# Kernel optimization log

Hardware: AMD Instinct MI355X
Metric: run time of the kernel (lower is better)

## Reference

```python
import jax, jax.numpy as jnp
import numpy as np

B, T, D = 8, 768, 1024
H = 16
DH = D // H  # 64, RoPE dim per head
ROPE_BASE = 10000.0


def _rope_tables(length, dim, dtype):
    # (T, dim) cos/sin tables, rotate-half convention
    inv_freq = 1.0 / (ROPE_BASE ** (jnp.arange(0, dim, 2, dtype=jnp.float32) / dim))
    ang = jnp.arange(length, dtype=jnp.float32)[:, None] * inv_freq[None, :]  # (T, dim/2)
    cos = jnp.concatenate([jnp.cos(ang), jnp.cos(ang)], axis=-1).astype(dtype)
    sin = jnp.concatenate([jnp.sin(ang), jnp.sin(ang)], axis=-1).astype(dtype)
    return cos, sin


def _rotate_half(x):
    half = x.shape[-1] // 2
    return jnp.concatenate([-x[..., half:], x[..., :half]], axis=-1)


def _apply_rope(x, cos, sin):
    # x: (B, H, T, DH); cos/sin: (T, DH)
    return x * cos[None, None] + _rotate_half(x) * sin[None, None]


def setup_inputs() -> dict:
    key = jax.random.key(0)
    kx, kw, kb = jax.random.split(key, 3)
    x = jax.random.normal(kx, (B, T, D), dtype=jnp.float32)
    bound = 1.0 / np.sqrt(D)
    W_qkv = jax.random.uniform(kw, (3 * D, D), dtype=jnp.float32, minval=-bound, maxval=bound)
    b_qkv = jax.random.uniform(kb, (3 * D,), dtype=jnp.float32, minval=-bound, maxval=bound)
    return {"x": x, "W_qkv": W_qkv, "b_qkv": b_qkv}


def reference(x, W_qkv, b_qkv):
    batch, length, dim = x.shape
    qkv = x @ W_qkv.T + b_qkv                      # (B, T, 3D)
    q, k, v = jnp.split(qkv, 3, axis=-1)
    # (B, T, D) -> (B, H, T, DH)
    def to_heads(t):
        return t.reshape(batch, length, H, DH).transpose(0, 2, 1, 3)
    q, k, v = to_heads(q), to_heads(k), to_heads(v)
    cos, sin = _rope_tables(length, DH, x.dtype)
    q = _apply_rope(q, cos, sin)
    k = _apply_rope(k, cos, sin)
    # parallel retention: QK^T (no softmax, no scale), causal mask multiply, @ V
    scores = jnp.einsum("bhtd,bhsd->bhts", q, k)   # (B, H, T, T)
    mask = jnp.tril(jnp.ones((length, length), dtype=x.dtype))
    retention = scores * mask[None, None]
    out = jnp.einsum("bhts,bhsd->bhtd", retention, v)  # (B, H, T, DH)
    return out.transpose(0, 2, 1, 3).reshape(batch, length, dim)
```

## Files before the change

kernel.cpp:

```cpp
#include <hip/hip_runtime.h>

#define B 8
#define T 768
#define D 1024
#define H 16
#define DH 64
#define M (B*T)
#define N3 (3*D)
#define KDIM D
#define QKV_ELEMS (B*H*T*DH)

typedef __attribute__((ext_vector_type(8))) short bf16x8;
typedef __attribute__((ext_vector_type(4))) short bf16x4;
typedef __attribute__((ext_vector_type(4))) float f32x4;

__device__ __forceinline__ unsigned short f2bf(float x) {
    union { float f; unsigned u; } a; a.f = x;
    unsigned r = a.u + 0x7FFFu + ((a.u >> 16) & 1u);
    return (unsigned short)(r >> 16);
}
__device__ __forceinline__ float bf2f(unsigned short h) {
    union { unsigned u; float f; } a; a.u = ((unsigned)h) << 16;
    return a.f;
}

__global__ void rope_tables_kernel(float* __restrict__ cosT, float* __restrict__ sinT) {
    int idx = blockIdx.x * blockDim.x + threadIdx.x;
    if (idx >= T * 32) return;
    int t = idx >> 5;
    int i = idx & 31;
    float inv_freq = powf(10000.0f, -(float)(2 * i) / 64.0f);
    float ang = (float)t * inv_freq;
    cosT[idx] = cosf(ang);
    sinT[idx] = sinf(ang);
}

#define BMq 128
#define BNq 128
#define BKq 32

__global__ __launch_bounds__(256) void qkv_mfma_kernel(
    const float* __restrict__ X, const float* __restrict__ W,
    const float* __restrict__ bias, const float* __restrict__ cosT,
    const float* __restrict__ sinT, float* __restrict__ qr,
    float* __restrict__ kr, float* __restrict__ vr)
{
    __shared__ unsigned short Ahi[BMq * BKq];
    __shared__ unsigned short Alo[BMq * BKq];
    __shared__ unsigned short Bhi[BNq * BKq];
    __shared__ unsigned short Blo[BNq * BKq];

    const int tid  = threadIdx.x;
    const int lane = tid & 63;
    const int w    = tid >> 6;
    const int wr   = w >> 1;
    const int wc   = w & 1;
    const int lr   = lane & 15;
    const int kc   = lane >> 4;

    const int m0 = blockIdx.x * BMq;
    const int n0 = blockIdx.y * BNq;

    const int srow = tid >> 1;
    const int kh   = tid & 1;

    f32x4 acc[4][4];
#pragma unroll
    for (int m = 0; m < 4; ++m)
#pragma unroll
        for (int n = 0; n < 4; ++n) acc[m][n] = (f32x4){0.f, 0.f, 0.f, 0.f};

    for (int k0 = 0; k0 < KDIM; k0 += BKq) {
        __syncthreads();
        {
            const float* src = X + (size_t)(m0 + srow) * KDIM + k0 + kh * 16;
            float v[16];
#pragma unroll
            for (int i = 0; i < 4; ++i) ((float4*)v)[i] = ((const float4*)src)[i];
#pragma unroll
            for (int c = 0; c < 2; ++c) {
                int chunk = kh * 2 + c;
                int sidx = srow * 32 + ((chunk ^ ((srow >> 1) & 3)) * 8);
                union { unsigned short u[8]; bf16x8 v8; } hiu, lou;
#pragma unroll
                for (int e = 0; e < 8; ++e) {
                    float x = v[c * 8 + e];
                    unsigned short h = f2bf(x);
                    hiu.u[e] = h;
                    lou.u[e] = f2bf(x - bf2f(h));
                }
                *(bf16x8*)&Ahi[sidx] = hiu.v8;
                *(bf16x8*)&Alo[sidx] = lou.v8;
            }
        }
        {
            const float* src = W + (size_t)(n0 + srow) * KDIM + k0 + kh * 16;
            float v[16];
#pragma unroll
            for (int i = 0; i < 4; ++i) ((float4*)v)[i] = ((const float4*)src)[i];
#pragma unroll
            for (int c = 0; c < 2; ++c) {
                int chunk = kh * 2 + c;
                int sidx = srow * 32 + ((chunk ^ ((srow >> 1) & 3)) * 8);
                union { unsigned short u[8]; bf16x8 v8; } hiu, lou;
#pragma unroll
                for (int e = 0; e < 8; ++e) {
                    float x = v[c * 8 + e];
                    unsigned short h = f2bf(x);
                    hiu.u[e] = h;
                    lou.u[e] = f2bf(x - bf2f(h));
                }
                *(bf16x8*)&Bhi[sidx] = hiu.v8;
                *(bf16x8*)&Blo[sidx] = lou.v8;
            }
        }
        __syncthreads();

        bf16x8 ah[4], al[4], bh[4], bl[4];
#pragma unroll
        for (int m = 0; m < 4; ++m) {
            int row = wr * 64 + m * 16 + lr;
            int idx = row * 32 + ((kc ^ ((row >> 1) & 3)) * 8);
            ah[m] = *(const bf16x8*)&Ahi[idx];
            al[m] = *(const bf16x8*)&Alo[idx];
        }
#pragma unroll
        for (int n = 0; n < 4; ++n) {
            int col = wc * 64 + n * 16 + lr;
            int idx = col * 32 + ((kc ^ ((col >> 1) & 3)) * 8);
            bh[n] = *(const bf16x8*)&Bhi[idx];
            bl[n] = *(const bf16x8*)&Blo[idx];
        }

#pragma unroll
        for (int m = 0; m < 4; ++m)
#pragma unroll
            for (int n = 0; n < 4; ++n) {
                acc[m][n] = __builtin_amdgcn_mfma_f32_16x16x32_bf16(ah[m], bh[n], acc[m][n], 0, 0, 0);
                acc[m][n] = __builtin_amdgcn_mfma_f32_16x16x32_bf16(ah[m], bl[n], acc[m][n], 0, 0, 0);
                acc[m][n] = __builtin_amdgcn_mfma_f32_16x16x32_bf16(al[m], bh[n], acc[m][n], 0, 0, 0);
            }
    }

    const int section = n0 >> 10;
    float* dst = (section == 0) ? qr : (section == 1) ? kr : vr;
    const int hcol = ((n0 & 1023) >> 6) + wc;

    float biasv[2][2];
#pragma unroll
    for (int np = 0; np < 2; ++np) {
        biasv[np][0] = bias[n0 + wc * 64 + np * 16 + lr];
        biasv[np][1] = bias[n0 + wc * 64 + np * 16 + lr + 32];
    }

#pragma unroll
    for (int m = 0; m < 4; ++m) {
#pragma unroll
        for (int j = 0; j < 4; ++j) {
            int grow = m0 + wr * 64 + m * 16 + (lane >> 4) * 4 + j;
            int bidx = grow / T;
            int t = grow - bidx * T;
            float* rowp = dst + (((size_t)bidx * H + hcol) * T + t) * DH;
#pragma unroll
            for (int np = 0; np < 2; ++np) {
                int d = np * 16 + lr;
                float vlo = acc[m][np][j]     + biasv[np][0];
                float vhi = acc[m][np + 2][j] + biasv[np][1];
                if (section < 2) {
                    float c = cosT[t * 32 + d];
                    float s = sinT[t * 32 + d];
                    float nl = vlo * c - vhi * s;
                    float nh = vhi * c + vlo * s;
                    vlo = nl; vhi = nh;
                }
                rowp[d]      = vlo;
                rowp[d + 32] = vhi;
            }
        }
    }
}

#define SBLK 64
#define QBLK 128
#define LDK 72

__global__ __launch_bounds__(256) void retention_mfma_kernel(
    const float* __restrict__ qr, const float* __restrict__ kr,
    const float* __restrict__ vr, float* __restrict__ out)
{
    __shared__ unsigned short Khi[SBLK * LDK], Klo[SBLK * LDK];
    __shared__ unsigned short Vthi[DH * LDK], Vtlo[DH * LDK];
    __shared__ unsigned short Shi[QBLK * LDK], Slo[QBLK * LDK];

    const int qb = blockIdx.x;
    const int bh = blockIdx.y;
    const int b = bh >> 4, h = bh & 15;
    const int tid = threadIdx.x;
    const int lane = tid & 63;
    const int w = tid >> 6;
    const int wm = w >> 1;
    const int wc = w & 1;
    const int lr = lane & 15;
    const int lg = lane >> 4;

    bf16x8 qh[4][2], ql[4][2];
    {
        const float* qp = qr + ((size_t)bh * T + (size_t)qb * QBLK + wm * 64) * DH;
#pragma unroll
        for (int m = 0; m < 4; ++m)
#pragma unroll
            for (int kk = 0; kk < 2; ++kk) {
                const float* p = qp + (m * 16 + lr) * DH + kk * 32 + lg * 8;
                float v[8];
                *(float4*)&v[0] = *(const float4*)p;
                *(float4*)&v[4] = *(const float4*)(p + 4);
                union { unsigned short u[8]; bf16x8 v8; } hu, lu;
#pragma unroll
                for (int e = 0; e < 8; ++e) {
                    unsigned short hv = f2bf(v[e]);
                    hu.u[e] = hv;
                    lu.u[e] = f2bf(v[e] - bf2f(hv));
                }
                qh[m][kk] = hu.v8;
                ql[m][kk] = lu.v8;
            }
    }

    f32x4 oacc[4][2];
#pragma unroll
    for (int m = 0; m < 4; ++m)
#pragma unroll
        for (int n = 0; n < 2; ++n) oacc[m][n] = (f32x4){0.f, 0.f, 0.f, 0.f};

    const int qmin = qb * QBLK + wm * 64;
    const int niter = 2 * qb + 2;

    for (int sb = 0; sb < niter; ++sb) {
        __syncthreads();
        {
            int row = tid >> 2, d0 = (tid & 3) * 16;
            const float* src = kr + ((size_t)bh * T + (size_t)sb * SBLK + row) * DH + d0;
            float v[16];
#pragma unroll
            for (int i = 0; i < 4; ++i) *(float4*)&v[i * 4] = *(const float4*)(src + i * 4);
#pragma unroll
            for (int c = 0; c < 2; ++c) {
                union { unsigned short u[8]; bf16x8 v8; } hu, lu;
#pragma unroll
                for (int e = 0; e < 8; ++e) {
                    float x = v[c * 8 + e];
                    unsigned short hv = f2bf(x);
                    hu.u[e] = hv;
                    lu.u[e] = f2bf(x - bf2f(hv));
                }
                int idx = row * LDK + d0 + c * 8;
                *(bf16x8*)&Khi[idx] = hu.v8;
                *(bf16x8*)&Klo[idx] = lu.v8;
            }
        }
        {
            int s0 = (tid >> 4) * 4, d0 = (tid & 15) * 4;
            const float* src = vr + ((size_t)bh * T + (size_t)sb * SBLK + s0) * DH + d0;
            float rv[4][4];
#pragma unroll
            for (int i = 0; i < 4; ++i) *(float4*)&rv[i][0] = *(const float4*)(src + (size_t)i * DH);
#pragma unroll
            for (int j = 0; j < 4; ++j) {
                union { unsigned short u[4]; bf16x4 v4; } hu, lu;
#pragma unroll
                for (int i = 0; i < 4; ++i) {
                    float x = rv[i][j];
                    unsigned short hv = f2bf(x);
                    hu.u[i] = hv;
                    lu.u[i] = f2bf(x - bf2f(hv));
                }
                int idx = (d0 + j) * LDK + s0;
                *(bf16x4*)&Vthi[idx] = hu.v4;
                *(bf16x4*)&Vtlo[idx] = lu.v4;
            }
        }
        __syncthreads();

        const bool active = (sb * SBLK <= qmin + 63);
        if (active) {
            f32x4 sacc[4][2];
#pragma unroll
            for (int m = 0; m < 4; ++m)
#pragma unroll
                for (int n = 0; n < 2; ++n) sacc[m][n] = (f32x4){0.f, 0.f, 0.f, 0.f};

#pragma unroll
            for (int kk = 0; kk < 2; ++kk) {
                bf16x8 kbh[2], kbl[2];
#pragma unroll
                for (int n = 0; n < 2; ++n) {
                    int s = wc * 32 + n * 16 + lr;
                    int idx = s * LDK + kk * 32 + lg * 8;
                    kbh[n] = *(const bf16x8*)&Khi[idx];
                    kbl[n] = *(const bf16x8*)&Klo[idx];
                }
#pragma unroll
                for (int m = 0; m < 4; ++m)
#pragma unroll
                    for (int n = 0; n < 2; ++n) {
                        sacc[m][n] = __builtin_amdgcn_mfma_f32_16x16x32_bf16(qh[m][kk], kbh[n], sacc[m][n], 0, 0, 0);
                        sacc[m][n] = __builtin_amdgcn_mfma_f32_16x16x32_bf16(qh[m][kk], kbl[n], sacc[m][n], 0, 0, 0);
                        sacc[m][n] = __builtin_amdgcn_mfma_f32_16x16x32_bf16(ql[m][kk], kbh[n], sacc[m][n], 0, 0, 0);
                    }
            }

            const bool needmask = (sb * SBLK + 63 > qmin);
#pragma unroll
            for (int m = 0; m < 4; ++m)
#pragma unroll
                for (int n = 0; n < 2; ++n) {
                    int sl = wc * 32 + n * 16 + lr;
                    int sg = sb * SBLK + sl;
#pragma unroll
                    for (int j = 0; j < 4; ++j) {
                        int rl = wm * 64 + m * 16 + lg * 4 + j;
                        int rg = qb * QBLK + rl;
                        float val = sacc[m][n][j];
                        if (needmask && sg > rg) val = 0.f;
                        unsigned short hv = f2bf(val);
                        int idx = rl * LDK + sl;
                        Shi[idx] = hv;
                        Slo[idx] = f2bf(val - bf2f(hv));
                    }
                }
        }
        __syncthreads();
        if (active) {
#pragma unroll
            for (int kk = 0; kk < 2; ++kk) {
                bf16x8 vbh[2], vbl[2], sah[4], sal[4];
#pragma unroll
                for (int n = 0; n < 2; ++n) {
                    int d = wc * 32 + n * 16 + lr;
                    int idx = d * LDK + kk * 32 + lg * 8;
                    vbh[n] = *(const bf16x8*)&Vthi[idx];
                    vbl[n] = *(const bf16x8*)&Vtlo[idx];
                }
#pragma unroll
                for (int m = 0; m < 4; ++m) {
                    int r = wm * 64 + m * 16 + lr;
                    int idx = r * LDK + kk * 32 + lg * 8;
                    sah[m] = *(const bf16x8*)&Shi[idx];
                    sal[m] = *(const bf16x8*)&Slo[idx];
                }
#pragma unroll
                for (int m = 0; m < 4; ++m)
#pragma unroll
                    for (int n = 0; n < 2; ++n) {
                        oacc[m][n] = __builtin_amdgcn_mfma_f32_16x16x32_bf16(sah[m], vbh[n], oacc[m][n], 0, 0, 0);
                        oacc[m][n] = __builtin_amdgcn_mfma_f32_16x16x32_bf16(sah[m], vbl[n], oacc[m][n], 0, 0, 0);
                        oacc[m][n] = __builtin_amdgcn_mfma_f32_16x16x32_bf16(sal[m], vbh[n], oacc[m][n], 0, 0, 0);
                    }
            }
        }
    }

#pragma unroll
    for (int m = 0; m < 4; ++m)
#pragma unroll
        for (int n = 0; n < 2; ++n) {
            int dcol = wc * 32 + n * 16 + lr;
#pragma unroll
            for (int j = 0; j < 4; ++j) {
                int t = qb * QBLK + wm * 64 + m * 16 + lg * 4 + j;
                out[((size_t)b * T + t) * D + h * DH + dcol] = oacc[m][n][j];
            }
        }
}

extern "C" void kernel_launch(void* const* d_in, const int* in_sizes, int n_in,
                              void* d_out, int out_size, void* d_ws, size_t ws_size,
                              hipStream_t stream) {
    const float* x    = (const float*)d_in[0];
    const float* Wq   = (const float*)d_in[1];
    const float* bq   = (const float*)d_in[2];
    float* out = (float*)d_out;
    float* ws  = (float*)d_ws;

    float* qr   = ws;
    float* kr   = ws + (size_t)QKV_ELEMS;
    float* vr   = ws + (size_t)2 * QKV_ELEMS;
    float* cosT = ws + (size_t)3 * QKV_ELEMS;
    float* sinT = cosT + T * 32;

    rope_tables_kernel<<<dim3((T * 32 + 255) / 256), dim3(256), 0, stream>>>(cosT, sinT);
    qkv_mfma_kernel<<<dim3(M / BMq, N3 / BNq), dim3(256), 0, stream>>>(
        x, Wq, bq, cosT, sinT, qr, kr, vr);
    retention_mfma_kernel<<<dim3(T / QBLK, B * H), dim3(256), 0, stream>>>(qr, kr, vr, out);
}
```

Measured before the change: 374.0 us.

## Pre-split QKV GEMM operands to bf16 hi/lo and stream via direct-to-LDS loads

Adds a pre-pass that converts x and W_qkv once into bf16 hi/lo pairs in the workspace. A new QKV GEMM kernel then loads these pre-split tiles with global_load_lds straight into swizzled shared memory. This removes the per-tile fp32-to-bf16 split conversion and register staging from the GEMM inner loop. In exchange it adds two conversion kernels, extra workspace traffic, and a fallback path when the workspace is too small.

```diff
diff --git a/kernel.cpp b/kernel.cpp
--- a/kernel.cpp
+++ b/kernel.cpp
@@ -9,6 +9,8 @@
 #define N3 (3*D)
 #define KDIM D
 #define QKV_ELEMS (B*H*T*DH)
+#define XE ((size_t)M * KDIM)
+#define WE ((size_t)N3 * KDIM)
 
 typedef __attribute__((ext_vector_type(8))) short bf16x8;
 typedef __attribute__((ext_vector_type(4))) short bf16x4;
@@ -22,6 +24,12 @@
 __device__ __forceinline__ float bf2f(unsigned short h) {
     union { unsigned u; float f; } a; a.u = ((unsigned)h) << 16;
     return a.f;
+}
+
+__device__ __forceinline__ void gload_lds16(const void* g, void* l) {
+    __builtin_amdgcn_global_load_lds(
+        (const __attribute__((address_space(1))) void*)g,
+        (__attribute__((address_space(3))) void*)l, 16, 0, 0);
 }
 
 __global__ void rope_tables_kernel(float* __restrict__ cosT, float* __restrict__ sinT) {
@@ -35,9 +43,138 @@
     sinT[idx] = sinf(ang);
 }
 
+__global__ __launch_bounds__(256) void split_convert_kernel(
+    const float* __restrict__ src, unsigned short* __restrict__ hi,
+    unsigned short* __restrict__ lo, int n8)
+{
+    int i = blockIdx.x * blockDim.x + threadIdx.x;
+    if (i >= n8) return;
+    const float* p = src + (size_t)i * 8;
+    float v[8];
+    *(float4*)&v[0] = ((const float4*)p)[0];
+    *(float4*)&v[4] = ((const float4*)p)[1];
+    union { unsigned short u[8]; uint4 q; } hu, lu;
+#pragma unroll
+    for (int e = 0; e < 8; ++e) {
+        unsigned short h = f2bf(v[e]);
+        hu.u[e] = h;
+        lu.u[e] = f2bf(v[e] - bf2f(h));
+    }
+    ((uint4*)hi)[i] = hu.q;
+    ((uint4*)lo)[i] = lu.q;
+}
+
 #define BMq 128
 #define BNq 128
 #define BKq 32
+
+__global__ __launch_bounds__(256) void qkv_mfma2_kernel(
+    const unsigned short* __restrict__ Xhi, const unsigned short* __restrict__ Xlo,
+    const unsigned short* __restrict__ Whi, const unsigned short* __restrict__ Wlo,
+    const float* __restrict__ bias, const float* __restrict__ cosT,
+    const float* __restrict__ sinT, float* __restrict__ qr,
+    float* __restrict__ kr, float* __restrict__ vr)
+{
+    __shared__ unsigned short Ah[BMq * BKq], Al[BMq * BKq];
+    __shared__ unsigned short Bh[BNq * BKq], Bl[BNq * BKq];
+
+    const int tid  = threadIdx.x;
+    const int lane = tid & 63;
+    const int w    = tid >> 6;
+    const int wr   = w >> 1;
+    const int wc   = w & 1;
+    const int lr   = lane & 15;
+    const int kc   = lane >> 4;
+
+    const int m0 = blockIdx.x * BMq;
+    const int n0 = blockIdx.y * BNq;
+
+    f32x4 acc[4][4];
+#pragma unroll
+    for (int m = 0; m < 4; ++m)
+#pragma unroll
+        for (int n = 0; n < 4; ++n) acc[m][n] = (f32x4){0.f, 0.f, 0.f, 0.f};
+
+    for (int k0 = 0; k0 < KDIM; k0 += BKq) {
+        __syncthreads();
+#pragma unroll
+        for (int i = 0; i < 2; ++i) {
+            int c   = w * 128 + i * 64 + lane;
+            int row = c >> 2;
+            int qq  = (c & 3) ^ ((row >> 2) & 3);
+            size_t goffA = (size_t)(m0 + row) * KDIM + k0 + qq * 8;
+            size_t goffB = (size_t)(n0 + row) * KDIM + k0 + qq * 8;
+            int lbase = (w * 128 + i * 64) * 8;
+            gload_lds16(Xhi + goffA, &Ah[lbase]);
+            gload_lds16(Xlo + goffA, &Al[lbase]);
+            gload_lds16(Whi + goffB, &Bh[lbase]);
+            gload_lds16(Wlo + goffB, &Bl[lbase]);
+        }
+        __syncthreads();
+
+        bf16x8 ah[4], al[4], bh[4], bl[4];
+#pragma unroll
+        for (int m = 0; m < 4; ++m) {
+            int r = wr * 64 + m * 16 + lr;
+            int idx = r * 32 + (kc ^ ((r >> 2) & 3)) * 8;
+            ah[m] = *(const bf16x8*)&Ah[idx];
+            al[m] = *(const bf16x8*)&Al[idx];
+        }
+#pragma unroll
+        for (int n = 0; n < 4; ++n) {
+            int ccol = wc * 64 + n * 16 + lr;
+            int idx = ccol * 32 + (kc ^ ((ccol >> 2) & 3)) * 8;
+            bh[n] = *(const bf16x8*)&Bh[idx];
+            bl[n] = *(const bf16x8*)&Bl[idx];
+        }
+
+#pragma unroll
+        for (int m = 0; m < 4; ++m)
+#pragma unroll
+            for (int n = 0; n < 4; ++n) {
+                acc[m][n] = __builtin_amdgcn_mfma_f32_16x16x32_bf16(ah[m], bh[n], acc[m][n], 0, 0, 0);
+                acc[m][n] = __builtin_amdgcn_mfma_f32_16x16x32_bf16(ah[m], bl[n], acc[m][n], 0, 0, 0);
+                acc[m][n] = __builtin_amdgcn_mfma_f32_16x16x32_bf16(al[m], bh[n], acc[m][n], 0, 0, 0);
+            }
+    }
+
+    const int section = n0 >> 10;
+    float* dst = (section == 0) ? qr : (section == 1) ? kr : vr;
+    const int hcol = ((n0 & 1023) >> 6) + wc;
+
+    float biasv[2][2];
+#pragma unroll
+    for (int np = 0; np < 2; ++np) {
+        biasv[np][0] = bias[n0 + wc * 64 + np * 16 + lr];
+        biasv[np][1] = bias[n0 + wc * 64 + np * 16 + lr + 32];
+    }
+
+#pragma unroll
+    for (int m = 0; m < 4; ++m) {
+#pragma unroll
+        for (int j = 0; j < 4; ++j) {
+            int grow = m0 + wr * 64 + m * 16 + (lane >> 4) * 4 + j;
+            int bidx = grow / T;
+            int t = grow - bidx * T;
+            float* rowp = dst + (((size_t)bidx * H + hcol) * T + t) * DH;
+#pragma unroll
+            for (int np = 0; np < 2; ++np) {
+                int d = np * 16 + lr;
+                float vlo = acc[m][np][j]     + biasv[np][0];
+                float vhi = acc[m][np + 2][j] + biasv[np][1];
+                if (section < 2) {
+                    float c = cosT[t * 32 + d];
+                    float s = sinT[t * 32 + d];
+                    float nl = vlo * c - vhi * s;
+                    float nh = vhi * c + vlo * s;
+                    vlo = nl; vhi = nh;
+                }
+                rowp[d]      = vlo;
+                rowp[d + 32] = vhi;
+            }
+        }
+    }
+}
 
 __global__ __launch_bounds__(256) void qkv_mfma_kernel(
     const float* __restrict__ X, const float* __restrict__ W,
@@ -388,8 +525,24 @@
     float* cosT = ws + (size_t)3 * QKV_ELEMS;
     float* sinT = cosT + T * 32;
 
+    const size_t float_bytes = ((size_t)3 * QKV_ELEMS + 2 * T * 32) * sizeof(float);
+    unsigned short* Xhi = (unsigned short*)((char*)d_ws + float_bytes);
+    unsigned short* Xlo = Xhi + XE;
+    unsigned short* Whi = Xlo + XE;
+    unsigned short* Wlo = Whi + WE;
+    const size_t need = float_bytes + (2 * XE + 2 * WE) * sizeof(unsigned short);
+
     rope_tables_kernel<<<dim3((T * 32 + 255) / 256), dim3(256), 0, stream>>>(cosT, sinT);
-    qkv_mfma_kernel<<<dim3(M / BMq, N3 / BNq), dim3(256), 0, stream>>>(
-        x, Wq, bq, cosT, sinT, qr, kr, vr);
+
+    if (ws_size >= need) {
+        split_convert_kernel<<<dim3((int)(XE / 8 / 256)), dim3(256), 0, stream>>>(x,  Xhi, Xlo, (int)(XE / 8));
+        split_convert_kernel<<<dim3((int)(WE / 8 / 256)), dim3(256), 0, stream>>>(Wq, Whi, Wlo, (int)(WE / 8));
+        qkv_mfma2_kernel<<<dim3(M / BMq, N3 / BNq), dim3(256), 0, stream>>>(
+            Xhi, Xlo, Whi, Wlo, bq, cosT, sinT, qr, kr, vr);
+    } else {
+        qkv_mfma_kernel<<<dim3(M / BMq, N3 / BNq), dim3(256), 0, stream>>>(
+            x, Wq, bq, cosT, sinT, qr, kr, vr);
+    }
+
     retention_mfma_kernel<<<dim3(T / QBLK, B * H), dim3(256), 0, stream>>>(qr, kr, vr, out);
 }
```

After: 338.1 us. 9.6% less time.

## Pre-split inputs to bf16 hi/lo and load GEMM tiles via global_load_lds

Applied to the files above, without the earlier changes.

Adds a separate pass that converts X and W once into bf16 hi/lo arrays, so the QKV GEMM no longer repeats the fp32-to-bf16 split in every tile iteration. The GEMM now streams tiles straight into LDS with global_load_lds. The QKV kernel also writes Q, K and V already split into hi/lo bf16, so the retention kernel can load them directly and use direct-to-LDS loads for K with a swizzled layout. The cost is two extra conversion launches plus extra workspace and memory traffic for the split copies.

```diff
diff --git a/kernel.cpp b/kernel.cpp
--- a/kernel.cpp
+++ b/kernel.cpp
@@ -9,6 +9,8 @@
 #define N3 (3*D)
 #define KDIM D
 #define QKV_ELEMS (B*H*T*DH)
+#define XE ((size_t)M * KDIM)
+#define WE ((size_t)N3 * KDIM)
 
 typedef __attribute__((ext_vector_type(8))) short bf16x8;
 typedef __attribute__((ext_vector_type(4))) short bf16x4;
@@ -22,6 +24,12 @@
 __device__ __forceinline__ float bf2f(unsigned short h) {
     union { unsigned u; float f; } a; a.u = ((unsigned)h) << 16;
     return a.f;
+}
+
+__device__ __forceinline__ void gload_lds16(const void* g, void* l) {
+    __builtin_amdgcn_global_load_lds(
+        (const __attribute__((address_space(1))) void*)g,
+        (__attribute__((address_space(3))) void*)l, 16, 0, 0);
 }
 
 __global__ void rope_tables_kernel(float* __restrict__ cosT, float* __restrict__ sinT) {
@@ -35,20 +43,42 @@
     sinT[idx] = sinf(ang);
 }
 
+__global__ __launch_bounds__(256) void split_convert_kernel(
+    const float* __restrict__ src, unsigned short* __restrict__ hi,
+    unsigned short* __restrict__ lo, int n8)
+{
+    int i = blockIdx.x * blockDim.x + threadIdx.x;
+    if (i >= n8) return;
+    const float* p = src + (size_t)i * 8;
+    float v[8];
+    *(float4*)&v[0] = ((const float4*)p)[0];
+    *(float4*)&v[4] = ((const float4*)p)[1];
+    union { unsigned short u[8]; uint4 q; } hu, lu;
+#pragma unroll
+    for (int e = 0; e < 8; ++e) {
+        unsigned short h = f2bf(v[e]);
+        hu.u[e] = h;
+        lu.u[e] = f2bf(v[e] - bf2f(h));
+    }
+    ((uint4*)hi)[i] = hu.q;
+    ((uint4*)lo)[i] = lu.q;
+}
+
 #define BMq 128
 #define BNq 128
 #define BKq 32
 
-__global__ __launch_bounds__(256) void qkv_mfma_kernel(
-    const float* __restrict__ X, const float* __restrict__ W,
+__global__ __launch_bounds__(256) void qkv_mfma2_kernel(
+    const unsigned short* __restrict__ Xhi, const unsigned short* __restrict__ Xlo,
+    const unsigned short* __restrict__ Whi, const unsigned short* __restrict__ Wlo,
     const float* __restrict__ bias, const float* __restrict__ cosT,
-    const float* __restrict__ sinT, float* __restrict__ qr,
-    float* __restrict__ kr, float* __restrict__ vr)
+    const float* __restrict__ sinT,
+    unsigned short* __restrict__ qhi, unsigned short* __restrict__ qlo,
+    unsigned short* __restrict__ khi, unsigned short* __restrict__ klo,
+    unsigned short* __restrict__ vhi, unsigned short* __restrict__ vlo)
 {
-    __shared__ unsigned short Ahi[BMq * BKq];
-    __shared__ unsigned short Alo[BMq * BKq];
-    __shared__ unsigned short Bhi[BNq * BKq];
-    __shared__ unsigned short Blo[BNq * BKq];
+    __shared__ unsigned short Ah[BMq * BKq], Al[BMq * BKq];
+    __shared__ unsigned short Bh[BNq * BKq], Bl[BNq * BKq];
 
     const int tid  = threadIdx.x;
     const int lane = tid & 63;
@@ -61,9 +91,6 @@
     const int m0 = blockIdx.x * BMq;
     const int n0 = blockIdx.y * BNq;
 
-    const int srow = tid >> 1;
-    const int kh   = tid & 1;
-
     f32x4 acc[4][4];
 #pragma unroll
     for (int m = 0; m < 4; ++m)
@@ -72,64 +99,35 @@
 
     for (int k0 = 0; k0 < KDIM; k0 += BKq) {
         __syncthreads();
-        {
-            const float* src = X + (size_t)(m0 + srow) * KDIM + k0 + kh * 16;
-            float v[16];
-#pragma unroll
-            for (int i = 0; i < 4; ++i) ((float4*)v)[i] = ((const float4*)src)[i];
-#pragma unroll
-            for (int c = 0; c < 2; ++c) {
-                int chunk = kh * 2 + c;
-                int sidx = srow * 32 + ((chunk ^ ((srow >> 1) & 3)) * 8);
-                union { unsigned short u[8]; bf16x8 v8; } hiu, lou;
-#pragma unroll
-                for (int e = 0; e < 8; ++e) {
-                    float x = v[c * 8 + e];
-                    unsigned short h = f2bf(x);
-                    hiu.u[e] = h;
-                    lou.u[e] = f2bf(x - bf2f(h));
-                }
-                *(bf16x8*)&Ahi[sidx] = hiu.v8;
-                *(bf16x8*)&Alo[sidx] = lou.v8;
-            }
-        }
-        {
-            const float* src = W + (size_t)(n0 + srow) * KDIM + k0 + kh * 16;
-            float v[16];
-#pragma unroll
-            for (int i = 0; i < 4; ++i) ((float4*)v)[i] = ((const float4*)src)[i];
-#pragma unroll
-            for (int c = 0; c < 2; ++c) {
-                int chunk = kh * 2 + c;
-                int sidx = srow * 32 + ((chunk ^ ((srow >> 1) & 3)) * 8);
-                union { unsigned short u[8]; bf16x8 v8; } hiu, lou;
-#pragma unroll
-                for (int e = 0; e < 8; ++e) {
-                    float x = v[c * 8 + e];
-                    unsigned short h = f2bf(x);
-                    hiu.u[e] = h;
-                    lou.u[e] = f2bf(x - bf2f(h));
-                }
-                *(bf16x8*)&Bhi[sidx] = hiu.v8;
-                *(bf16x8*)&Blo[sidx] = lou.v8;
-            }
+#pragma unroll
+        for (int i = 0; i < 2; ++i) {
+            int c   = w * 128 + i * 64 + lane;
+            int row = c >> 2;
+            int qq  = (c & 3) ^ ((row >> 1) & 3);
+            size_t goffA = (size_t)(m0 + row) * KDIM + k0 + qq * 8;
+            size_t goffB = (size_t)(n0 + row) * KDIM + k0 + qq * 8;
+            int lbase = (w * 128 + i * 64) * 8;
+            gload_lds16(Xhi + goffA, &Ah[lbase]);
+            gload_lds16(Xlo + goffA, &Al[lbase]);
+            gload_lds16(Whi + goffB, &Bh[lbase]);
+            gload_lds16(Wlo + goffB, &Bl[lbase]);
         }
         __syncthreads();
 
         bf16x8 ah[4], al[4], bh[4], bl[4];
 #pragma unroll
         for (int m = 0; m < 4; ++m) {
-            int row = wr * 64 + m * 16 + lr;
-            int idx = row * 32 + ((kc ^ ((row >> 1) & 3)) * 8);
-            ah[m] = *(const bf16x8*)&Ahi[idx];
-            al[m] = *(const bf16x8*)&Alo[idx];
+            int r = wr * 64 + m * 16 + lr;
+            int idx = r * 32 + (kc ^ ((r >> 1) & 3)) * 8;
+            ah[m] = *(const bf16x8*)&Ah[idx];
+            al[m] = *(const bf16x8*)&Al[idx];
         }
 #pragma unroll
         for (int n = 0; n < 4; ++n) {
-            int col = wc * 64 + n * 16 + lr;
-            int idx = col * 32 + ((kc ^ ((col >> 1) & 3)) * 8);
-            bh[n] = *(const bf16x8*)&Bhi[idx];
-            bl[n] = *(const bf16x8*)&Blo[idx];
+            int ccol = wc * 64 + n * 16 + lr;
+            int idx = ccol * 32 + (kc ^ ((ccol >> 1) & 3)) * 8;
+            bh[n] = *(const bf16x8*)&Bh[idx];
+            bl[n] = *(const bf16x8*)&Bl[idx];
         }
 
 #pragma unroll
@@ -143,7 +141,8 @@
     }
 
     const int section = n0 >> 10;
-    float* dst = (section == 0) ? qr : (section == 1) ? kr : vr;
+    unsigned short* dhi = (section == 0) ? qhi : (section == 1) ? khi : vhi;
+    unsigned short* dlo = (section == 0) ? qlo : (section == 1) ? klo : vlo;
     const int hcol = ((n0 & 1023) >> 6) + wc;
 
     float biasv[2][2];
@@ -160,21 +159,25 @@
             int grow = m0 + wr * 64 + m * 16 + (lane >> 4) * 4 + j;
             int bidx = grow / T;
             int t = grow - bidx * T;
-            float* rowp = dst + (((size_t)bidx * H + hcol) * T + t) * DH;
+            size_t rowbase = (((size_t)bidx * H + hcol) * T + t) * DH;
 #pragma unroll
             for (int np = 0; np < 2; ++np) {
                 int d = np * 16 + lr;
-                float vlo = acc[m][np][j]     + biasv[np][0];
-                float vhi = acc[m][np + 2][j] + biasv[np][1];
+                float vlo_ = acc[m][np][j]     + biasv[np][0];
+                float vhi_ = acc[m][np + 2][j] + biasv[np][1];
                 if (section < 2) {
                     float c = cosT[t * 32 + d];
                     float s = sinT[t * 32 + d];
-                    float nl = vlo * c - vhi * s;
-                    float nh = vhi * c + vlo * s;
-                    vlo = nl; vhi = nh;
-                }
-                rowp[d]      = vlo;
-                rowp[d + 32] = vhi;
+                    float nl = vlo_ * c - vhi_ * s;
+                    float nh = vhi_ * c + vlo_ * s;
+                    vlo_ = nl; vhi_ = nh;
+                }
+                unsigned short h0 = f2bf(vlo_);
+                dhi[rowbase + d]      = h0;
+                dlo[rowbase + d]      = f2bf(vlo_ - bf2f(h0));
+                unsigned short h1 = f2bf(vhi_);
+                dhi[rowbase + d + 32] = h1;
+                dlo[rowbase + d + 32] = f2bf(vhi_ - bf2f(h1));
             }
         }
     }
@@ -185,11 +188,13 @@
 #define LDK 72
 
 __global__ __launch_bounds__(256) void retention_mfma_kernel(
-    const float* __restrict__ qr, const float* __restrict__ kr,
-    const float* __restrict__ vr, float* __restrict__ out)
+    const unsigned short* __restrict__ qhi, const unsigned short* __restrict__ qlo,
+    const unsigned short* __restrict__ khi, const unsigned short* __restrict__ klo,
+    const unsigned short* __restrict__ vhi, const unsigned short* __restrict__ vlo,
+    float* __restrict__ out)
 {
-    __shared__ unsigned short Khi[SBLK * LDK], Klo[SBLK * LDK];
-    __shared__ unsigned short Vthi[DH * LDK], Vtlo[DH * LDK];
+    __shared__ unsigned short Kh[SBLK * DH], Kl[SBLK * DH];
+    __shared__ unsigned short Vth[DH * LDK], Vtl[DH * LDK];
     __shared__ unsigned short Shi[QBLK * LDK], Slo[QBLK * LDK];
 
     const int qb = blockIdx.x;
@@ -205,24 +210,14 @@
 
     bf16x8 qh[4][2], ql[4][2];
     {
-        const float* qp = qr + ((size_t)bh * T + (size_t)qb * QBLK + wm * 64) * DH;
+        const size_t qbase = ((size_t)bh * T + (size_t)qb * QBLK + wm * 64) * DH;
 #pragma unroll
         for (int m = 0; m < 4; ++m)
 #pragma unroll
             for (int kk = 0; kk < 2; ++kk) {
-                const float* p = qp + (m * 16 + lr) * DH + kk * 32 + lg * 8;
-                float v[8];
-                *(float4*)&v[0] = *(const float4*)p;
-                *(float4*)&v[4] = *(const float4*)(p + 4);
-                union { unsigned short u[8]; bf16x8 v8; } hu, lu;
-#pragma unroll
-                for (int e = 0; e < 8; ++e) {
-                    unsigned short hv = f2bf(v[e]);
-                    hu.u[e] = hv;
-                    lu.u[e] = f2bf(v[e] - bf2f(hv));
-                }
-                qh[m][kk] = hu.v8;
-                ql[m][kk] = lu.v8;
+                size_t off = qbase + (size_t)(m * 16 + lr) * DH + kk * 32 + lg * 8;
+                qh[m][kk] = *(const bf16x8*)(qhi + off);
+                ql[m][kk] = *(const bf16x8*)(qlo + off);
             }
     }
 
@@ -237,46 +232,34 @@
 
     for (int sb = 0; sb < niter; ++sb) {
         __syncthreads();
-        {
-            int row = tid >> 2, d0 = (tid & 3) * 16;
-            const float* src = kr + ((size_t)bh * T + (size_t)sb * SBLK + row) * DH + d0;
-            float v[16];
-#pragma unroll
-            for (int i = 0; i < 4; ++i) *(float4*)&v[i * 4] = *(const float4*)(src + i * 4);
-#pragma unroll
-            for (int c = 0; c < 2; ++c) {
-                union { unsigned short u[8]; bf16x8 v8; } hu, lu;
-#pragma unroll
-                for (int e = 0; e < 8; ++e) {
-                    float x = v[c * 8 + e];
-                    unsigned short hv = f2bf(x);
-                    hu.u[e] = hv;
-                    lu.u[e] = f2bf(x - bf2f(hv));
-                }
-                int idx = row * LDK + d0 + c * 8;
-                *(bf16x8*)&Khi[idx] = hu.v8;
-                *(bf16x8*)&Klo[idx] = lu.v8;
-            }
+#pragma unroll
+        for (int i = 0; i < 2; ++i) {
+            int c    = w * 128 + i * 64 + lane;
+            int row  = c >> 3;
+            int slot = c & 7;
+            int cg   = slot ^ (row & 7);
+            size_t goff = ((size_t)bh * T + (size_t)sb * SBLK + row) * DH + cg * 8;
+            int lbase = (w * 128 + i * 64) * 8;
+            gload_lds16(khi + goff, &Kh[lbase]);
+            gload_lds16(klo + goff, &Kl[lbase]);
         }
         {
             int s0 = (tid >> 4) * 4, d0 = (tid & 15) * 4;
-            const float* src = vr + ((size_t)bh * T + (size_t)sb * SBLK + s0) * DH + d0;
-            float rv[4][4];
-#pragma unroll
-            for (int i = 0; i < 4; ++i) *(float4*)&rv[i][0] = *(const float4*)(src + (size_t)i * DH);
+            size_t vbase = ((size_t)bh * T + (size_t)sb * SBLK + s0) * DH + d0;
+            unsigned short rh[4][4], rl[4][4];
+#pragma unroll
+            for (int i = 0; i < 4; ++i) {
+                *(bf16x4*)&rh[i][0] = *(const bf16x4*)(vhi + vbase + (size_t)i * DH);
+                *(bf16x4*)&rl[i][0] = *(const bf16x4*)(vlo + vbase + (size_t)i * DH);
+            }
 #pragma unroll
             for (int j = 0; j < 4; ++j) {
-                union { unsigned short u[4]; bf16x4 v4; } hu, lu;
-#pragma unroll
-                for (int i = 0; i < 4; ++i) {
-                    float x = rv[i][j];
-                    unsigned short hv = f2bf(x);
-                    hu.u[i] = hv;
-                    lu.u[i] = f2bf(x - bf2f(hv));
-                }
+                union { unsigned short u[4]; bf16x4 v4; } th, tl;
+#pragma unroll
+                for (int i = 0; i < 4; ++i) { th.u[i] = rh[i][j]; tl.u[i] = rl[i][j]; }
                 int idx = (d0 + j) * LDK + s0;
-                *(bf16x4*)&Vthi[idx] = hu.v4;
-                *(bf16x4*)&Vtlo[idx] = lu.v4;
+                *(bf16x4*)&Vth[idx] = th.v4;
+                *(bf16x4*)&Vtl[idx] = tl.v4;
             }
         }
         __syncthreads();
@@ -295,9 +278,9 @@
 #pragma unroll
                 for (int n = 0; n < 2; ++n) {
                     int s = wc * 32 + n * 16 + lr;
-                    int idx = s * LDK + kk * 32 + lg * 8;
-                    kbh[n] = *(const bf16x8*)&Khi[idx];
-                    kbl[n] = *(const bf16x8*)&Klo[idx];
+                    int idx = s * 64 + ((kk * 4 + lg) ^ (s & 7)) * 8;
+                    kbh[n] = *(const bf16x8*)&Kh[idx];
+                    kbl[n] = *(const bf16x8*)&Kl[idx];
                 }
 #pragma unroll
                 for (int m = 0; m < 4; ++m)
@@ -318,12 +301,12 @@
                     int sg = sb * SBLK + sl;
 #pragma unroll
                     for (int j = 0; j < 4; ++j) {
-                        int rl = wm * 64 + m * 16 + lg * 4 + j;
-                        int rg = qb * QBLK + rl;
+                        int rl_ = wm * 64 + m * 16 + lg * 4 + j;
+                        int rg = qb * QBLK + rl_;
                         float val = sacc[m][n][j];
                         if (needmask && sg > rg) val = 0.f;
                         unsigned short hv = f2bf(val);
-                        int idx = rl * LDK + sl;
+                        int idx = rl_ * LDK + sl;
                         Shi[idx] = hv;
                         Slo[idx] = f2bf(val - bf2f(hv));
                     }
@@ -338,8 +321,8 @@
                 for (int n = 0; n < 2; ++n) {
                     int d = wc * 32 + n * 16 + lr;
                     int idx = d * LDK + kk * 32 + lg * 8;
-                    vbh[n] = *(const bf16x8*)&Vthi[idx];
-                    vbl[n] = *(const bf16x8*)&Vtlo[idx];
+                    vbh[n] = *(const bf16x8*)&Vth[idx];
+                    vbl[n] = *(const bf16x8*)&Vtl[idx];
                 }
 #pragma unroll
                 for (int m = 0; m < 4; ++m) {
@@ -380,16 +363,25 @@
     const float* Wq   = (const float*)d_in[1];
     const float* bq   = (const float*)d_in[2];
     float* out = (float*)d_out;
-    float* ws  = (float*)d_ws;
-
-    float* qr   = ws;
-    float* kr   = ws + (size_t)QKV_ELEMS;
-    float* vr   = ws + (size_t)2 * QKV_ELEMS;
-    float* cosT = ws + (size_t)3 * QKV_ELEMS;
+
+    unsigned short* qhi = (unsigned short*)d_ws;
+    unsigned short* qlo = qhi + QKV_ELEMS;
+    unsigned short* khi = qlo + QKV_ELEMS;
+    unsigned short* klo = khi + QKV_ELEMS;
+    unsigned short* vhi = klo + QKV_ELEMS;
+    unsigned short* vlo = vhi + QKV_ELEMS;
+    float* cosT = (float*)(vlo + QKV_ELEMS);
     float* sinT = cosT + T * 32;
+    unsigned short* Xhi = (unsigned short*)(sinT + T * 32);
+    unsigned short* Xlo = Xhi + XE;
+    unsigned short* Whi = Xlo + XE;
+    unsigned short* Wlo = Whi + WE;
 
     rope_tables_kernel<<<dim3((T * 32 + 255) / 256), dim3(256), 0, stream>>>(cosT, sinT);
-    qkv_mfma_kernel<<<dim3(M / BMq, N3 / BNq), dim3(256), 0, stream>>>(
-        x, Wq, bq, cosT, sinT, qr, kr, vr);
-    retention_mfma_kernel<<<dim3(T / QBLK, B * H), dim3(256), 0, stream>>>(qr, kr, vr, out);
-}
+    split_convert_kernel<<<dim3((int)(XE / 8 / 256)), dim3(256), 0, stream>>>(x,  Xhi, Xlo, (int)(XE / 8));
+    split_convert_kernel<<<dim3((int)(WE / 8 / 256)), dim3(256), 0, stream>>>(Wq, Whi, Wlo, (int)(WE / 8));
+    qkv_mfma2_kernel<<<dim3(M / BMq, N3 / BNq), dim3(256), 0, stream>>>(
+        Xhi, Xlo, Whi, Wlo, bq, cosT, sinT, qhi, qlo, khi, klo, vhi, vlo);
+    retention_mfma_kernel<<<dim3(T / QBLK, B * H), dim3(256), 0, stream>>>(
+        qhi, qlo, khi, klo, vhi, vlo, out);
+}
```

Measured after the change: 343.1 us. -8.3%, faster.
